# Kernel tuning notes

Hardware: AMD Instinct MI355X
Metric: run time of the kernel (lower is better)

Reference implementation:

```python
import jax, jax.numpy as jnp
import numpy as np


def setup_inputs() -> dict:
    key = jax.random.key(0)
    ks = jax.random.split(key, 6)
    B, C, H, W = 4, 512, 64, 64
    Ci = C // 2
    x = jax.random.normal(ks[0], (B, C, H, W), dtype=jnp.float32)
    # 1x1 conv weights (kaiming-ish scale)
    wq = jax.random.normal(ks[1], (Ci, C), dtype=jnp.float32) * np.float32(np.sqrt(2.0 / C))
    wk = jax.random.normal(ks[2], (Ci, C), dtype=jnp.float32) * np.float32(np.sqrt(2.0 / C))
    wv = jax.random.normal(ks[3], (C, C), dtype=jnp.float32) * np.float32(np.sqrt(2.0 / C))
    bq = jnp.zeros((Ci,), jnp.float32)
    bk = jnp.zeros((Ci,), jnp.float32)
    bv = jnp.zeros((C,), jnp.float32)
    gamma_pam = jax.random.uniform(ks[4], (1,), dtype=jnp.float32)
    gamma_cam = jax.random.uniform(ks[5], (1,), dtype=jnp.float32)
    return {"x": x, "wq": wq, "bq": bq, "wk": wk, "bk": bk,
            "wv": wv, "bv": bv, "gamma_pam": gamma_pam, "gamma_cam": gamma_cam}


def reference(x, wq, bq, wk, bk, wv, bv, gamma_pam, gamma_cam):
    B, C, H, W = x.shape
    N = H * W
    xf = x.reshape(B, C, N)  # [B,C,N]

    # ---- PAM (position attention) ----
    q = jnp.einsum('oc,bcn->bon', wq, xf) + bq[None, :, None]  # [B,C/2,N]
    k = jnp.einsum('oc,bcn->bon', wk, xf) + bk[None, :, None]  # [B,C/2,N]
    v = jnp.einsum('oc,bcn->bon', wv, xf) + bv[None, :, None]  # [B,C,N]
    # energy[b,i,j] = sum_c q[b,c,i] k[b,c,j] / sqrt(C)
    energy = jnp.einsum('bci,bcj->bij', q, k) / jnp.sqrt(jnp.float32(C))
    attn = jax.nn.softmax(energy, axis=-1) / jnp.float32(N)  # [B,N,N]
    # out[b,c,i] = sum_j v[b,c,j] * attn[i,j]
    pam_out = jnp.einsum('bcj,bij->bci', v, attn)
    sa = jnp.tanh(gamma_pam[0] * pam_out + xf)  # [B,C,N]

    # ---- CAM (channel attention) on sa ----
    energy_c = jnp.einsum('bcn,bdn->bcd', sa, sa) / jnp.sqrt(jnp.float32(N))  # [B,C,C]
    energy_new = jnp.max(energy_c, axis=-1, keepdims=True) - energy_c
    attn_c = jax.nn.softmax(energy_new, axis=-1) / jnp.float32(C)
    cam_out = jnp.einsum('bcd,bdn->bcn', attn_c, sa)
    out = gamma_cam[0] * cam_out + sa
    return out.reshape(B, C, H, W)
```

## Files before the change

kernel.cpp:

```cpp
#include <hip/hip_runtime.h>

#define B_ 4
#define C_ 512
#define CI_ 256
#define N_ 4096
#define SCALE_PAM 0.04419417382415922f
#define SCALE_CAM (1.0f/64.0f)
#define SHIFT_PAM 8.0f

typedef float v4f __attribute__((ext_vector_type(4)));
typedef short v8s __attribute__((ext_vector_type(8)));

__device__ __forceinline__ unsigned short f2bf(float f) {
  unsigned int u = __float_as_uint(f);
  u = (u + 0x7FFFu + ((u >> 16) & 1u)) >> 16;
  return (unsigned short)u;
}
__device__ __forceinline__ float bf2f(unsigned short s) {
  return __uint_as_float(((unsigned int)s) << 16);
}
__device__ __forceinline__ v8s ld8(const unsigned short* p) {
  v8s r; *(int4*)&r = *(const int4*)p; return r;
}
__device__ __forceinline__ v4f mfma16(v8s a, v8s b, v4f c) {
  return __builtin_amdgcn_mfma_f32_16x16x32_bf16(a, b, c, 0, 0, 0);
}

__global__ __launch_bounds__(256) void k_wb(const float* __restrict__ wq,
                                            const float* __restrict__ wk,
                                            const float* __restrict__ wv,
                                            unsigned short* __restrict__ w_pk) {
  int u = blockIdx.x * 256 + threadIdx.x;
  int blk = u >> 6, wi = (u & 63) * 8;
  int r = (blk >> 4) * 16 + (wi >> 5);
  int k = (blk & 15) * 32 + (wi & 31);
  const float* src = (r < 256) ? &wq[r * 512 + k]
                   : (r < 512) ? &wk[(r - 256) * 512 + k]
                               : &wv[(r - 512) * 512 + k];
  float4 f0 = *(const float4*)src, f1 = *(const float4*)(src + 4);
  ushort4 o0 = { f2bf(f0.x), f2bf(f0.y), f2bf(f0.z), f2bf(f0.w) };
  ushort4 o1 = { f2bf(f1.x), f2bf(f1.y), f2bf(f1.z), f2bf(f1.w) };
  *(ushort4*)&w_pk[u * 8] = o0;
  *(ushort4*)&w_pk[u * 8 + 4] = o1;
}

__global__ __launch_bounds__(256) void k_xT(const float* __restrict__ x,
                                            unsigned short* __restrict__ x_pk) {
  const int b = blockIdx.z, c0 = blockIdx.y * 64, n0 = blockIdx.x * 64;
  const int t = threadIdx.x;
  __shared__ unsigned short ts[64 * 72];
  const int cl = t >> 2, nseg = (t & 3) * 16;
  const float* xr = x + ((size_t)b * C_ + c0 + cl) * N_ + n0 + nseg;
#pragma unroll
  for (int k = 0; k < 4; ++k) {
    float4 f = *(const float4*)(xr + k * 4);
    ts[(nseg + k * 4 + 0) * 72 + cl] = f2bf(f.x);
    ts[(nseg + k * 4 + 1) * 72 + cl] = f2bf(f.y);
    ts[(nseg + k * 4 + 2) * 72 + cl] = f2bf(f.z);
    ts[(nseg + k * 4 + 3) * 72 + cl] = f2bf(f.w);
  }
  __syncthreads();
  unsigned short* dst = x_pk + (size_t)b * N_ * C_;
#pragma unroll
  for (int u = t; u < 512; u += 256) {
    int blk = u >> 6, wi = (u & 63) * 8;
    int rl = (blk >> 1) * 16 + (wi >> 5);
    int kl = (blk & 1) * 32 + (wi & 31);
    int gr = n0 + rl, gk = c0 + kl;
    size_t go = ((size_t)(gr >> 4) * 16 + (gk >> 5)) * 512 + (gr & 15) * 32 + (gk & 31);
    *(int4*)&dst[go] = *(int4*)&ts[rl * 72 + kl];
  }
}

__global__ __launch_bounds__(512) void k_qkv(
    const unsigned short* __restrict__ w_pk, const unsigned short* __restrict__ x_pk,
    const float* __restrict__ bq, const float* __restrict__ bk, const float* __restrict__ bv,
    unsigned short* __restrict__ q_pk, unsigned short* __restrict__ k_pk,
    unsigned short* __restrict__ v_pk) {
  const int b = blockIdx.z, o0 = blockIdx.y * 128, n0 = blockIdx.x * 128;
  const int t = threadIdx.x, wave = t >> 6, lane = t & 63;
  const int la = lane & 15, quad = lane >> 4;
  const int ow = wave & 1, nw = wave >> 1;
  const int lanelin = la * 32 + quad * 8;
  const unsigned short* xpb = x_pk + (size_t)b * N_ * C_;
  __shared__ unsigned short tp[128 * 136];

  v4f acc[4][2];
#pragma unroll
  for (int i = 0; i < 4; ++i)
#pragma unroll
    for (int j = 0; j < 2; ++j) acc[i][j] = (v4f){0.f, 0.f, 0.f, 0.f};

  const int ar16 = (o0 + ow * 64) >> 4;
  const int br16 = (n0 + nw * 32) >> 4;
#pragma unroll 4
  for (int s = 0; s < 16; ++s) {
    v8s b0 = ld8(&xpb[((size_t)(br16 + 0) * 16 + s) * 512 + lanelin]);
    v8s b1 = ld8(&xpb[((size_t)(br16 + 1) * 16 + s) * 512 + lanelin]);
#pragma unroll
    for (int oi = 0; oi < 4; ++oi) {
      v8s a = ld8(&w_pk[((size_t)(ar16 + oi) * 16 + s) * 512 + lanelin]);
      acc[oi][0] = mfma16(a, b0, acc[oi][0]);
      acc[oi][1] = mfma16(a, b1, acc[oi][1]);
    }
  }

  if (o0 >= 512) {
#pragma unroll
    for (int oi = 0; oi < 4; ++oi)
#pragma unroll
      for (int nj = 0; nj < 2; ++nj)
#pragma unroll
        for (int r = 0; r < 4; ++r) {
          int cl = ow * 64 + oi * 16 + quad * 4 + r;
          int nl = nw * 32 + nj * 16 + la;
          tp[cl * 136 + nl] = f2bf(acc[oi][nj][r] + bv[o0 - 512 + cl]);
        }
    __syncthreads();
    unsigned short* dst = v_pk + (size_t)b * C_ * N_;
#pragma unroll
    for (int u = t; u < 2048; u += 512) {
      int blk = u >> 6, wi = (u & 63) * 8;
      int rl = (blk >> 2) * 16 + (wi >> 5);
      int kl = (blk & 3) * 32 + (wi & 31);
      int gr = (o0 - 512) + rl, gk = n0 + kl;
      size_t go = ((size_t)(gr >> 4) * 128 + (gk >> 5)) * 512 + (gr & 15) * 32 + (gk & 31);
      *(int4*)&dst[go] = *(int4*)&tp[rl * 136 + kl];
    }
  } else {
    const float* bias = (o0 < 256) ? bq : bk;
#pragma unroll
    for (int oi = 0; oi < 4; ++oi)
#pragma unroll
      for (int nj = 0; nj < 2; ++nj)
#pragma unroll
        for (int r = 0; r < 4; ++r) {
          int ol = ow * 64 + oi * 16 + quad * 4 + r;
          int nl = nw * 32 + nj * 16 + la;
          tp[nl * 136 + ol] = f2bf(acc[oi][nj][r] + bias[(o0 & 255) + ol]);
        }
    __syncthreads();
    unsigned short* dst = ((o0 < 256) ? q_pk : k_pk) + (size_t)b * N_ * CI_;
#pragma unroll
    for (int u = t; u < 2048; u += 512) {
      int blk = u >> 6, wi = (u & 63) * 8;
      int rl = (blk >> 2) * 16 + (wi >> 5);
      int kl = (blk & 3) * 32 + (wi & 31);
      int gr = n0 + rl, gk = (o0 & 255) + kl;
      size_t go = ((size_t)(gr >> 4) * 8 + (gk >> 5)) * 512 + (gr & 15) * 32 + (gk & 31);
      *(int4*)&dst[go] = *(int4*)&tp[rl * 136 + kl];
    }
  }
}

__device__ __forceinline__ void kstage512(const unsigned short* g, unsigned short* l, int t) {
#pragma unroll
  for (int u = 0; u < 4; ++u)
    __builtin_amdgcn_global_load_lds(
        (const __attribute__((address_space(1))) void*)(g + (size_t)(u * 512 + t) * 8),
        (__attribute__((address_space(3))) void*)(l + (u * 512 + t) * 8), 16, 0, 0);
}

__global__ __launch_bounds__(512, 2) void k_pam(
    const unsigned short* __restrict__ q_pk, const unsigned short* __restrict__ k_pk,
    const unsigned short* __restrict__ v_pk,
    float* __restrict__ acc_part, float* __restrict__ l_part) {
  const int blk = blockIdx.x;
  const int b = (blk & 7) >> 1, jh = blk & 1, i0 = (blk >> 3) * 64;
  const int t = threadIdx.x, wave = t >> 6, lane = t & 63;
  const int la = lane & 15, quad = lane >> 4;
  const int iw = wave & 1, jw = wave >> 1;
  const int cb = wave * 64;
  const int lanelin = la * 32 + quad * 8;

  __shared__ unsigned short kls[3][16384];
  __shared__ unsigned short pa[2][4096];
  __shared__ float l_lds[64];
  if (t < 64) l_lds[t] = 0.f;

  const unsigned short* qpk = q_pk + (size_t)b * N_ * CI_;
  const unsigned short* kpk = k_pk + (size_t)b * N_ * CI_;
  const unsigned short* vpk = v_pk + (size_t)b * C_ * N_;

  v8s qf[16];
#pragma unroll
  for (int rb = 0; rb < 2; ++rb) {
    const unsigned short* qb = qpk + ((size_t)((i0 >> 4) + iw * 2 + rb) * 8) * 512 + lanelin;
#pragma unroll
    for (int s = 0; s < 8; ++s) qf[rb * 8 + s] = ld8(qb + s * 512);
  }

  v4f acc[4][4];
#pragma unroll
  for (int ct = 0; ct < 4; ++ct)
#pragma unroll
    for (int it = 0; it < 4; ++it) acc[ct][it] = (v4f){0.f, 0.f, 0.f, 0.f};
  float lsum[2][4] = {{0.f, 0.f, 0.f, 0.f}, {0.f, 0.f, 0.f, 0.f}};

  const int jbeg = jh * 2048, jend = jbeg + 2048;
  kstage512(kpk + (size_t)(jbeg >> 4) * 4096, kls[0], t);
  kstage512(kpk + (size_t)((jbeg + 64) >> 4) * 4096, kls[1], t);
  asm volatile("s_waitcnt vmcnt(4)" ::: "memory");
  __builtin_amdgcn_s_barrier();
  __builtin_amdgcn_sched_barrier(0);

  int pb = 0;
  for (int step = 0; step < 32; ++step) {
    const int j0 = jbeg + step * 64;
    v8s vf[4][2];
#pragma unroll
    for (int ct = 0; ct < 4; ++ct)
#pragma unroll
      for (int ks = 0; ks < 2; ++ks)
        vf[ct][ks] = ld8(&vpk[((size_t)((cb >> 4) + ct) * 128 + (j0 >> 5) + ks) * 512 + lanelin]);
    __builtin_amdgcn_sched_barrier(0);
    int jn = j0 + 128; if (jn >= jend) jn = jbeg;
    kstage512(kpk + (size_t)(jn >> 4) * 4096, kls[(step + 2) % 3], t);
    __builtin_amdgcn_sched_barrier(0);
    {
      const unsigned short* kb = &kls[step % 3][jw * 4096 + lanelin];
      v8s kf[8];
#pragma unroll
      for (int s = 0; s < 8; ++s) kf[s] = ld8(kb + s * 512);
#pragma unroll
      for (int is2 = 0; is2 < 2; ++is2) {
        v4f sA = (v4f){0.f, 0.f, 0.f, 0.f}, sB = sA;
#pragma unroll
        for (int sh = 0; sh < 4; ++sh) {
          sA = mfma16(qf[is2 * 8 + sh], kf[sh], sA);
          sB = mfma16(qf[is2 * 8 + 4 + sh], kf[4 + sh], sB);
        }
#pragma unroll
        for (int r = 0; r < 4; ++r) {
          float p = __expf((sA[r] + sB[r]) * SCALE_PAM - SHIFT_PAM);
          lsum[is2][r] += p;
          int row = iw * 32 + is2 * 16 + quad * 4 + r;
          pa[pb][((row << 6) + jw * 16 + la) ^ ((row & 7) << 3)] = f2bf(p);
        }
      }
    }
    __builtin_amdgcn_sched_barrier(0);
    asm volatile("s_waitcnt lgkmcnt(0) vmcnt(12)" ::: "memory");
    __builtin_amdgcn_s_barrier();
    __builtin_amdgcn_sched_barrier(0);
    __builtin_amdgcn_s_setprio(1);
#pragma unroll
    for (int it = 0; it < 4; ++it) {
      const int row = it * 16 + la;
      const int sw = (row & 7) << 3;
#pragma unroll
      for (int ks = 0; ks < 2; ++ks) {
        v8s pf; *(int4*)&pf = *(const int4*)&pa[pb][((row << 6) + ks * 32 + quad * 8) ^ sw];
#pragma unroll
        for (int ct = 0; ct < 4; ++ct)
          acc[ct][it] = mfma16(vf[ct][ks], pf, acc[ct][it]);
      }
    }
    __builtin_amdgcn_s_setprio(0);
    pb ^= 1;
  }

#pragma unroll
  for (int is2 = 0; is2 < 2; ++is2)
#pragma unroll
    for (int r = 0; r < 4; ++r) {
      float v = lsum[is2][r];
      v += __shfl_xor(v, 1); v += __shfl_xor(v, 2);
      v += __shfl_xor(v, 4); v += __shfl_xor(v, 8);
      if (la == 0) atomicAdd(&l_lds[iw * 32 + is2 * 16 + quad * 4 + r], v);
    }
  __syncthreads();
  if (t < 64) l_part[((size_t)jh * B_ + b) * N_ + i0 + t] = l_lds[t];

  float* ap = acc_part + ((size_t)jh * B_ + b) * C_ * N_;
#pragma unroll
  for (int ct = 0; ct < 4; ++ct)
#pragma unroll
    for (int it = 0; it < 4; ++it)
#pragma unroll
      for (int r = 0; r < 4; ++r)
        ap[(size_t)(cb + ct * 16 + quad * 4 + r) * N_ + i0 + it * 16 + la] = acc[ct][it][r];
}

__global__ __launch_bounds__(256) void k_combine(
    const float* __restrict__ acc_part, const float* __restrict__ l_part,
    const float* __restrict__ x, const float* __restrict__ gamma_pam,
    unsigned short* __restrict__ sa_pk, unsigned short* __restrict__ saT_pk) {
  const int b = blockIdx.z, c0 = blockIdx.y * 64, n0 = blockIdx.x * 64;
  const int t = threadIdx.x;
  const int cl = t >> 2, nseg = (t & 3) * 16;
  __shared__ unsigned short ts[64 * 72];
  const float gpv = gamma_pam[0];
  const size_t rowoff = ((size_t)b * C_ + c0 + cl) * N_ + n0 + nseg;
  const float* a0 = acc_part + rowoff;
  const float* a1 = acc_part + (size_t)B_ * C_ * N_ + rowoff;
  const float* xr = x + rowoff;
  const float* l0 = l_part + (size_t)b * N_ + n0 + nseg;
  const float* l1 = l_part + ((size_t)B_ + b) * N_ + n0 + nseg;
  unsigned short sv[16];
#pragma unroll
  for (int k = 0; k < 4; ++k) {
    float4 p4 = *(const float4*)(a0 + k * 4);
    float4 q4 = *(const float4*)(a1 + k * 4);
    float4 x4 = *(const float4*)(xr + k * 4);
    float4 u4 = *(const float4*)(l0 + k * 4);
    float4 w4 = *(const float4*)(l1 + k * 4);
    sv[k * 4 + 0] = f2bf(tanhf(fmaf(gpv, (p4.x + q4.x) / ((u4.x + w4.x) * (float)N_), x4.x)));
    sv[k * 4 + 1] = f2bf(tanhf(fmaf(gpv, (p4.y + q4.y) / ((u4.y + w4.y) * (float)N_), x4.y)));
    sv[k * 4 + 2] = f2bf(tanhf(fmaf(gpv, (p4.z + q4.z) / ((u4.z + w4.z) * (float)N_), x4.z)));
    sv[k * 4 + 3] = f2bf(tanhf(fmaf(gpv, (p4.w + q4.w) / ((u4.w + w4.w) * (float)N_), x4.w)));
  }
#pragma unroll
  for (int k = 0; k < 16; ++k) ts[cl * 72 + nseg + k] = sv[k];
  __syncthreads();
  {
    unsigned short* dst = sa_pk + (size_t)b * C_ * N_;
#pragma unroll
    for (int u = t; u < 512; u += 256) {
      int blk = u >> 6, wi = (u & 63) * 8;
      int rl = (blk >> 1) * 16 + (wi >> 5);
      int kl = (blk & 1) * 32 + (wi & 31);
      int gr = c0 + rl, gk = n0 + kl;
      size_t go = ((size_t)(gr >> 4) * 128 + (gk >> 5)) * 512 + (gr & 15) * 32 + (gk & 31);
      *(int4*)&dst[go] = *(int4*)&ts[rl * 72 + kl];
    }
  }
  __syncthreads();
#pragma unroll
  for (int k = 0; k < 16; ++k) ts[(nseg + k) * 72 + cl] = sv[k];
  __syncthreads();
  {
    unsigned short* dst = saT_pk + (size_t)b * N_ * C_;
#pragma unroll
    for (int u = t; u < 512; u += 256) {
      int blk = u >> 6, wi = (u & 63) * 8;
      int rl = (blk >> 1) * 16 + (wi >> 5);
      int kl = (blk & 1) * 32 + (wi & 31);
      int gr = n0 + rl, gk = c0 + kl;
      size_t go = ((size_t)(gr >> 4) * 16 + (gk >> 5)) * 512 + (gr & 15) * 32 + (gk & 31);
      *(int4*)&dst[go] = *(int4*)&ts[rl * 72 + kl];
    }
  }
}

__global__ __launch_bounds__(256) void k_cam_e(const unsigned short* __restrict__ sa_pk,
                                               float* __restrict__ e_part) {
  const int b = blockIdx.z, ks = blockIdx.y;
  const int c0 = (blockIdx.x & 7) * 64, d0 = (blockIdx.x >> 3) * 64;
  const int t = threadIdx.x, wave = t >> 6, lane = t & 63;
  const int la = lane & 15, quad = lane >> 4;
  const int cw = wave & 1, dw = wave >> 1;
  const int lanelin = la * 32 + quad * 8;
  const unsigned short* sb = sa_pk + (size_t)b * C_ * N_;

  v4f acc[2][2];
#pragma unroll
  for (int i = 0; i < 2; ++i)
#pragma unroll
    for (int j = 0; j < 2; ++j) acc[i][j] = (v4f){0.f, 0.f, 0.f, 0.f};

  const int ar16 = (c0 + cw * 32) >> 4;
  const int br16 = (d0 + dw * 32) >> 4;
#pragma unroll 4
  for (int s = 0; s < 32; ++s) {
    const int k32 = ks * 32 + s;
    v8s a0 = ld8(&sb[((size_t)(ar16 + 0) * 128 + k32) * 512 + lanelin]);
    v8s a1 = ld8(&sb[((size_t)(ar16 + 1) * 128 + k32) * 512 + lanelin]);
    v8s b0 = ld8(&sb[((size_t)(br16 + 0) * 128 + k32) * 512 + lanelin]);
    v8s b1 = ld8(&sb[((size_t)(br16 + 1) * 128 + k32) * 512 + lanelin]);
    acc[0][0] = mfma16(a0, b0, acc[0][0]);
    acc[0][1] = mfma16(a0, b1, acc[0][1]);
    acc[1][0] = mfma16(a1, b0, acc[1][0]);
    acc[1][1] = mfma16(a1, b1, acc[1][1]);
  }
  float* ep = e_part + ((size_t)(ks * B_ + b)) * C_ * C_;
#pragma unroll
  for (int i = 0; i < 2; ++i)
#pragma unroll
    for (int j = 0; j < 2; ++j)
#pragma unroll
      for (int r = 0; r < 4; ++r) {
        int c = c0 + cw * 32 + i * 16 + quad * 4 + r;
        int d = d0 + dw * 32 + j * 16 + la;
        ep[(size_t)c * C_ + d] = acc[i][j][r] * SCALE_CAM;
      }
}

__global__ __launch_bounds__(64) void k_cam_softmax(const float* __restrict__ e_part,
                                                    unsigned short* __restrict__ attn_pk) {
  const int c = blockIdx.x, b = blockIdx.y, lane = threadIdx.x;
  size_t roff = ((size_t)b * C_ + c) * C_;
  float vals[8];
#pragma unroll
  for (int r = 0; r < 8; ++r) {
    int d = lane + r * 64;
    float s = 0.f;
#pragma unroll
    for (int p = 0; p < 4; ++p) s += e_part[(size_t)(p * B_) * C_ * C_ + roff + d];
    vals[r] = s;
  }
  float mn = vals[0];
#pragma unroll
  for (int r = 1; r < 8; ++r) mn = fminf(mn, vals[r]);
#pragma unroll
  for (int m = 32; m >= 1; m >>= 1) mn = fminf(mn, __shfl_xor(mn, m));
  float sum = 0.f;
#pragma unroll
  for (int r = 0; r < 8; ++r) { vals[r] = __expf(mn - vals[r]); sum += vals[r]; }
#pragma unroll
  for (int m = 32; m >= 1; m >>= 1) sum += __shfl_xor(sum, m);
  float sc = (1.0f / (float)C_) / sum;
  unsigned short* ab = attn_pk + (size_t)b * C_ * C_;
#pragma unroll
  for (int r = 0; r < 8; ++r) {
    int d = lane + r * 64;
    size_t go = ((size_t)(c >> 4) * 16 + (d >> 5)) * 512 + (c & 15) * 32 + (d & 31);
    ab[go] = f2bf(vals[r] * sc);
  }
}

__global__ __launch_bounds__(512) void k_cam_out(
    const unsigned short* __restrict__ attn_pk, const unsigned short* __restrict__ saT_pk,
    const unsigned short* __restrict__ sa_pk, const float* __restrict__ gamma_cam,
    float* __restrict__ out) {
  const int b = blockIdx.z, c0 = blockIdx.y * 128, n0 = blockIdx.x * 128;
  const int t = threadIdx.x, wave = t >> 6, lane = t & 63;
  const int la = lane & 15, quad = lane >> 4;
  const int cw = wave & 1, nw = wave >> 1;
  const int lanelin = la * 32 + quad * 8;
  const unsigned short* ab = attn_pk + (size_t)b * C_ * C_;
  const unsigned short* sTb = saT_pk + (size_t)b * N_ * C_;
  const unsigned short* sb = sa_pk + (size_t)b * C_ * N_;

  v4f acc[4][2];
#pragma unroll
  for (int i = 0; i < 4; ++i)
#pragma unroll
    for (int j = 0; j < 2; ++j) acc[i][j] = (v4f){0.f, 0.f, 0.f, 0.f};

  const int ar16 = (c0 + cw * 64) >> 4;
  const int br16 = (n0 + nw * 32) >> 4;
#pragma unroll 4
  for (int s = 0; s < 16; ++s) {
    v8s b0 = ld8(&sTb[((size_t)(br16 + 0) * 16 + s) * 512 + lanelin]);
    v8s b1 = ld8(&sTb[((size_t)(br16 + 1) * 16 + s) * 512 + lanelin]);
#pragma unroll
    for (int ci = 0; ci < 4; ++ci) {
      v8s a = ld8(&ab[((size_t)(ar16 + ci) * 16 + s) * 512 + lanelin]);
      acc[ci][0] = mfma16(a, b0, acc[ci][0]);
      acc[ci][1] = mfma16(a, b1, acc[ci][1]);
    }
  }
  const float gc = gamma_cam[0];
#pragma unroll
  for (int ci = 0; ci < 4; ++ci)
#pragma unroll
    for (int nj = 0; nj < 2; ++nj)
#pragma unroll
      for (int r = 0; r < 4; ++r) {
        int c = c0 + cw * 64 + ci * 16 + quad * 4 + r;
        int n = n0 + nw * 32 + nj * 16 + la;
        size_t pko = ((size_t)(c >> 4) * 128 + (n >> 5)) * 512 + (c & 15) * 32 + (n & 31);
        out[((size_t)b * C_ + c) * N_ + n] = fmaf(gc, acc[ci][nj][r], bf2f(sb[pko]));
      }
}

extern "C" void kernel_launch(void* const* d_in, const int* in_sizes, int n_in,
                              void* d_out, int out_size, void* d_ws, size_t ws_size,
                              hipStream_t stream) {
  const float* x  = (const float*)d_in[0];
  const float* wq = (const float*)d_in[1];
  const float* bq = (const float*)d_in[2];
  const float* wk = (const float*)d_in[3];
  const float* bk = (const float*)d_in[4];
  const float* wv = (const float*)d_in[5];
  const float* bv = (const float*)d_in[6];
  const float* gp = (const float*)d_in[7];
  const float* gc = (const float*)d_in[8];
  float* out = (float*)d_out;

  char* ws = (char*)d_ws;
  unsigned short* x_pk   = (unsigned short*)(ws);
  unsigned short* w_pk   = (unsigned short*)(ws + 16777216);
  unsigned short* q_pk   = (unsigned short*)(ws + 17825792);
  unsigned short* k_pk   = (unsigned short*)(ws + 26214400);
  unsigned short* v_pk   = (unsigned short*)(ws + 34603008);
  float*          acc_p  = (float*)(ws + 51380224);
  float*          l_p    = (float*)(ws + 118489088);
  unsigned short* sa_pk  = (unsigned short*)(ws);
  unsigned short* saT_pk = (unsigned short*)(ws + 17825792);
  float*          ep     = (float*)(ws + 34603008);
  unsigned short* at_pk  = (unsigned short*)(ws + 51380224);

  k_xT<<<dim3(64, 8, B_), 256, 0, stream>>>(x, x_pk);
  k_wb<<<256, 256, 0, stream>>>(wq, wk, wv, w_pk);
  k_qkv<<<dim3(32, 8, B_), 512, 0, stream>>>(w_pk, x_pk, bq, bk, bv, q_pk, k_pk, v_pk);
  k_pam<<<512, 512, 0, stream>>>(q_pk, k_pk, v_pk, acc_p, l_p);
  k_combine<<<dim3(64, 8, B_), 256, 0, stream>>>(acc_p, l_p, x, gp, sa_pk, saT_pk);
  k_cam_e<<<dim3(64, 4, B_), 256, 0, stream>>>(sa_pk, ep);
  k_cam_softmax<<<dim3(C_, B_), 64, 0, stream>>>(ep, at_pk);
  k_cam_out<<<dim3(32, 4, B_), 512, 0, stream>>>(at_pk, saT_pk, sa_pk, gc, out);
}
```

Before: 403.4 us.

## Warp-specialize PAM kernel into score producers and PV consumer waves

The PAM attention kernel is split into four producer waves and four consumer waves. Producers compute the QK scores, exp and bf16 P tile for step i+1, while consumers run the PV MFMAs for step i into a wider 128-channel accumulator per wave. K staging drops from triple to double buffering, and each step now ends with a full block barrier. Each half of the block does only one kind of work, so the MFMA load is uneven and the per-wave register footprint grows.

Measured after the change: 435.3 us. 7.9% more time.

```diff
diff --git a/kernel.cpp b/kernel.cpp
--- a/kernel.cpp
+++ b/kernel.cpp
@@ -161,6 +161,34 @@
         (__attribute__((address_space(3))) void*)(l + (u * 512 + t) * 8), 16, 0, 0);
 }
 
+__device__ __forceinline__ void s_phase(const unsigned short* kslot, unsigned short* patile,
+                                        const v4f (&u)[32], float (&lsum)[2][4],
+                                        int iw, int jw, int la, int quad, int lanelin) {
+#pragma unroll
+  for (int js2 = 0; js2 < 2; ++js2) {
+    const unsigned short* kb = kslot + (jw * 2 + js2) * 4096 + lanelin;
+    v8s kfb[8];
+#pragma unroll
+    for (int s = 0; s < 8; ++s) kfb[s] = ld8(kb + s * 512);
+#pragma unroll
+    for (int is2 = 0; is2 < 2; ++is2) {
+      v4f sA = (v4f){0.f, 0.f, 0.f, 0.f}, sB = sA;
+#pragma unroll
+      for (int sh = 0; sh < 4; ++sh) {
+        sA = mfma16(__builtin_bit_cast(v8s, u[is2 * 8 + sh]), kfb[sh], sA);
+        sB = mfma16(__builtin_bit_cast(v8s, u[is2 * 8 + 4 + sh]), kfb[4 + sh], sB);
+      }
+#pragma unroll
+      for (int r = 0; r < 4; ++r) {
+        float p = __expf((sA[r] + sB[r]) * SCALE_PAM - SHIFT_PAM);
+        lsum[is2][r] += p;
+        int row = iw * 32 + is2 * 16 + quad * 4 + r;
+        patile[((row << 6) + (jw * 2 + js2) * 16 + la) ^ ((row & 7) << 3)] = f2bf(p);
+      }
+    }
+  }
+}
+
 __global__ __launch_bounds__(512, 2) void k_pam(
     const unsigned short* __restrict__ q_pk, const unsigned short* __restrict__ k_pk,
     const unsigned short* __restrict__ v_pk,
@@ -169,11 +197,12 @@
   const int b = (blk & 7) >> 1, jh = blk & 1, i0 = (blk >> 3) * 64;
   const int t = threadIdx.x, wave = t >> 6, lane = t & 63;
   const int la = lane & 15, quad = lane >> 4;
-  const int iw = wave & 1, jw = wave >> 1;
-  const int cb = wave * 64;
+  const bool prod = wave < 4;
+  const int iw = wave & 1, jw = (wave >> 1) & 1;
+  const int cw = wave - 4, cb = cw * 128;
   const int lanelin = la * 32 + quad * 8;
 
-  __shared__ unsigned short kls[3][16384];
+  __shared__ unsigned short kls[2][16384];
   __shared__ unsigned short pa[2][4096];
   __shared__ float l_lds[64];
   if (t < 64) l_lds[t] = 0.f;
@@ -182,104 +211,87 @@
   const unsigned short* kpk = k_pk + (size_t)b * N_ * CI_;
   const unsigned short* vpk = v_pk + (size_t)b * C_ * N_;
 
-  v8s qf[16];
-#pragma unroll
-  for (int rb = 0; rb < 2; ++rb) {
-    const unsigned short* qb = qpk + ((size_t)((i0 >> 4) + iw * 2 + rb) * 8) * 512 + lanelin;
-#pragma unroll
-    for (int s = 0; s < 8; ++s) qf[rb * 8 + s] = ld8(qb + s * 512);
-  }
-
-  v4f acc[4][4];
-#pragma unroll
-  for (int ct = 0; ct < 4; ++ct)
-#pragma unroll
-    for (int it = 0; it < 4; ++it) acc[ct][it] = (v4f){0.f, 0.f, 0.f, 0.f};
-  float lsum[2][4] = {{0.f, 0.f, 0.f, 0.f}, {0.f, 0.f, 0.f, 0.f}};
-
-  const int jbeg = jh * 2048, jend = jbeg + 2048;
+  v4f u[32];
+  float lsum[2][4];
+
+  const int jbeg = jh * 2048;
+
   kstage512(kpk + (size_t)(jbeg >> 4) * 4096, kls[0], t);
   kstage512(kpk + (size_t)((jbeg + 64) >> 4) * 4096, kls[1], t);
-  asm volatile("s_waitcnt vmcnt(4)" ::: "memory");
-  __builtin_amdgcn_s_barrier();
-  __builtin_amdgcn_sched_barrier(0);
-
-  int pb = 0;
-  for (int step = 0; step < 32; ++step) {
-    const int j0 = jbeg + step * 64;
-    v8s vf[4][2];
-#pragma unroll
-    for (int ct = 0; ct < 4; ++ct)
-#pragma unroll
-      for (int ks = 0; ks < 2; ++ks)
-        vf[ct][ks] = ld8(&vpk[((size_t)((cb >> 4) + ct) * 128 + (j0 >> 5) + ks) * 512 + lanelin]);
-    __builtin_amdgcn_sched_barrier(0);
-    int jn = j0 + 128; if (jn >= jend) jn = jbeg;
-    kstage512(kpk + (size_t)(jn >> 4) * 4096, kls[(step + 2) % 3], t);
-    __builtin_amdgcn_sched_barrier(0);
-    {
-      const unsigned short* kb = &kls[step % 3][jw * 4096 + lanelin];
-      v8s kf[8];
-#pragma unroll
-      for (int s = 0; s < 8; ++s) kf[s] = ld8(kb + s * 512);
-#pragma unroll
-      for (int is2 = 0; is2 < 2; ++is2) {
-        v4f sA = (v4f){0.f, 0.f, 0.f, 0.f}, sB = sA;
-#pragma unroll
-        for (int sh = 0; sh < 4; ++sh) {
-          sA = mfma16(qf[is2 * 8 + sh], kf[sh], sA);
-          sB = mfma16(qf[is2 * 8 + 4 + sh], kf[4 + sh], sB);
-        }
-#pragma unroll
-        for (int r = 0; r < 4; ++r) {
-          float p = __expf((sA[r] + sB[r]) * SCALE_PAM - SHIFT_PAM);
-          lsum[is2][r] += p;
-          int row = iw * 32 + is2 * 16 + quad * 4 + r;
-          pa[pb][((row << 6) + jw * 16 + la) ^ ((row & 7) << 3)] = f2bf(p);
+  if (prod) {
+#pragma unroll
+    for (int rb = 0; rb < 2; ++rb) {
+      const unsigned short* qb = qpk + ((size_t)((i0 >> 4) + iw * 2 + rb) * 8) * 512 + lanelin;
+#pragma unroll
+      for (int s = 0; s < 8; ++s) u[rb * 8 + s] = __builtin_bit_cast(v4f, ld8(qb + s * 512));
+    }
+#pragma unroll
+    for (int is2 = 0; is2 < 2; ++is2)
+#pragma unroll
+      for (int r = 0; r < 4; ++r) lsum[is2][r] = 0.f;
+  } else {
+#pragma unroll
+    for (int z = 0; z < 32; ++z) u[z] = (v4f){0.f, 0.f, 0.f, 0.f};
+  }
+  __syncthreads();
+
+  if (prod) s_phase(kls[0], pa[0], u, lsum, iw, jw, la, quad, lanelin);
+  __syncthreads();
+
+  for (int i = 0; i < 32; ++i) {
+    if (i < 30)
+      kstage512(kpk + (size_t)((jbeg + (i + 2) * 64) >> 4) * 4096, kls[i & 1], t);
+    if (prod) {
+      if (i < 31) s_phase(kls[(i + 1) & 1], pa[(i + 1) & 1], u, lsum, iw, jw, la, quad, lanelin);
+    } else {
+      const int j0 = jbeg + i * 64;
+      v8s vf[8][2];
+#pragma unroll
+      for (int ct = 0; ct < 8; ++ct)
+#pragma unroll
+        for (int ks = 0; ks < 2; ++ks)
+          vf[ct][ks] = ld8(&vpk[((size_t)((cb >> 4) + ct) * 128 + (j0 >> 5) + ks) * 512 + lanelin]);
+      __builtin_amdgcn_s_setprio(1);
+#pragma unroll
+      for (int it = 0; it < 4; ++it) {
+        const int row = it * 16 + la;
+        const int sw = (row & 7) << 3;
+#pragma unroll
+        for (int ks = 0; ks < 2; ++ks) {
+          v8s pf; *(int4*)&pf = *(const int4*)&pa[i & 1][((row << 6) + ks * 32 + quad * 8) ^ sw];
+#pragma unroll
+          for (int ct = 0; ct < 8; ++ct)
+            u[ct * 4 + it] = mfma16(vf[ct][ks], pf, u[ct * 4 + it]);
         }
       }
-    }
-    __builtin_amdgcn_sched_barrier(0);
-    asm volatile("s_waitcnt lgkmcnt(0) vmcnt(12)" ::: "memory");
-    __builtin_amdgcn_s_barrier();
-    __builtin_amdgcn_sched_barrier(0);
-    __builtin_amdgcn_s_setprio(1);
-#pragma unroll
-    for (int it = 0; it < 4; ++it) {
-      const int row = it * 16 + la;
-      const int sw = (row & 7) << 3;
-#pragma unroll
-      for (int ks = 0; ks < 2; ++ks) {
-        v8s pf; *(int4*)&pf = *(const int4*)&pa[pb][((row << 6) + ks * 32 + quad * 8) ^ sw];
-#pragma unroll
-        for (int ct = 0; ct < 4; ++ct)
-          acc[ct][it] = mfma16(vf[ct][ks], pf, acc[ct][it]);
+      __builtin_amdgcn_s_setprio(0);
+    }
+    __syncthreads();
+  }
+
+  if (prod) {
+#pragma unroll
+    for (int is2 = 0; is2 < 2; ++is2)
+#pragma unroll
+      for (int r = 0; r < 4; ++r) {
+        float v = lsum[is2][r];
+        v += __shfl_xor(v, 1); v += __shfl_xor(v, 2);
+        v += __shfl_xor(v, 4); v += __shfl_xor(v, 8);
+        if (la == 0) atomicAdd(&l_lds[iw * 32 + is2 * 16 + quad * 4 + r], v);
       }
-    }
-    __builtin_amdgcn_s_setprio(0);
-    pb ^= 1;
-  }
-
-#pragma unroll
-  for (int is2 = 0; is2 < 2; ++is2)
-#pragma unroll
-    for (int r = 0; r < 4; ++r) {
-      float v = lsum[is2][r];
-      v += __shfl_xor(v, 1); v += __shfl_xor(v, 2);
-      v += __shfl_xor(v, 4); v += __shfl_xor(v, 8);
-      if (la == 0) atomicAdd(&l_lds[iw * 32 + is2 * 16 + quad * 4 + r], v);
-    }
+  }
   __syncthreads();
   if (t < 64) l_part[((size_t)jh * B_ + b) * N_ + i0 + t] = l_lds[t];
-
-  float* ap = acc_part + ((size_t)jh * B_ + b) * C_ * N_;
-#pragma unroll
-  for (int ct = 0; ct < 4; ++ct)
-#pragma unroll
-    for (int it = 0; it < 4; ++it)
-#pragma unroll
-      for (int r = 0; r < 4; ++r)
-        ap[(size_t)(cb + ct * 16 + quad * 4 + r) * N_ + i0 + it * 16 + la] = acc[ct][it][r];
+  if (!prod) {
+    float* ap = acc_part + ((size_t)jh * B_ + b) * C_ * N_;
+#pragma unroll
+    for (int ct = 0; ct < 8; ++ct)
+#pragma unroll
+      for (int it = 0; it < 4; ++it)
+#pragma unroll
+        for (int r = 0; r < 4; ++r)
+          ap[(size_t)(cb + ct * 16 + quad * 4 + r) * N_ + i0 + it * 16 + la] = u[ct * 4 + it][r];
+  }
 }
 
 __global__ __launch_bounds__(256) void k_combine(
```
